# Performance work log

Measured on AMD Instinct MI355X. Metric: run time of the kernel, lower is better.

Reference implementation:

```python
import jax, jax.numpy as jnp
import numpy as np

B, S, D, H, DH = 2, 1024, 1024, 16, 64
SCALE = 1.0 / np.sqrt(DH)


def setup_inputs() -> dict:
    key = jax.random.key(0)
    ks = jax.random.split(key, 9)
    return {
        "x": jax.random.normal(ks[0], (B, S, D), jnp.float32),
        "qkv_w": jax.random.normal(ks[1], (3 * H * DH, D), jnp.float32) * 0.02,
        "out_w": jax.random.normal(ks[2], (D, H * DH), jnp.float32) * 0.02,
        "bias_p": jax.random.uniform(ks[3], (H, 1, 1), jnp.float32) * 2.0,
        "bias_a": jax.random.uniform(ks[4], (H, 1, 1), jnp.float32),
        "mlp_w1": jax.random.normal(ks[5], (H, 2 * H), jnp.float32) * 0.1,
        "mlp_b1": jnp.zeros((H,), jnp.float32),
        "mlp_w2": jax.random.normal(ks[6], (H, H), jnp.float32) * 0.1,
        "mlp_b2": jnp.zeros((H,), jnp.float32),
    }


def reference(x, qkv_w, out_w, bias_p, bias_a, mlp_w1, mlp_b1, mlp_w2, mlp_b2):
    # qkv projection: torch Linear => x @ W.T
    qkv = (x @ qkv_w.T).reshape(B, S, 3, H, DH)
    q = qkv[:, :, 0].transpose(0, 2, 1, 3)  # [B,H,S,DH]
    k = qkv[:, :, 1].transpose(0, 2, 1, 3)
    v = qkv[:, :, 2].transpose(0, 2, 1, 3)

    scores = jnp.einsum('bhqd,bhkd->bhqk', q, k) * SCALE  # [B,H,S,S]

    # Kerple additive bias: -p * log1p(a * |i-j|), per head
    p = jnp.clip(bias_p, 0.01)
    a = jnp.clip(bias_a, 0.01)
    pos = jnp.arange(S, dtype=jnp.float32)
    dist = jnp.abs(pos[None, :] - pos[:, None])  # [S,S]
    kb = -p * jnp.log1p(a * dist)  # [H,S,S]

    # DAPE refinement MLP over per-(i,j) head features
    z = jnp.concatenate(
        [scores, jnp.broadcast_to(kb[None], (B, H, S, S))], axis=1
    ).transpose(0, 2, 3, 1)  # [B,S,S,2H]
    hdn = jax.nn.gelu(z @ mlp_w1.T + mlp_b1, approximate=False)  # [B,S,S,H]
    refine = (hdn @ mlp_w2.T + mlp_b2).transpose(0, 3, 1, 2)  # [B,H,S,S]

    scores = scores + kb[None] + refine
    attn = jax.nn.softmax(scores, axis=-1)  # dropout is identity in eval

    out = jnp.einsum('bhqk,bhkd->bhqd', attn, v)  # [B,H,S,DH]
    out = out.transpose(0, 2, 1, 3).reshape(B, S, H * DH)
    return out @ out_w.T
```

## Files before the change

### kernel.cpp

```cpp
#include <hip/hip_runtime.h>
#include <math.h>

#define Bsz 2
#define Ssz 1024
#define Dsz 1024
#define Hn 16
#define DHsz 64
#define QKV3 3072
#define SCALE 0.125f

typedef __bf16 bf16;
typedef bf16 bf16x8 __attribute__((ext_vector_type(8)));
typedef bf16 bf16x4 __attribute__((ext_vector_type(4)));
typedef float f32x4 __attribute__((ext_vector_type(4)));

#define MFMA(a, b, c) __builtin_amdgcn_mfma_f32_16x16x32_bf16(a, b, c, 0, 0, 0)
#define LDT 72

__global__ void cast_all(const float* __restrict__ x, const float* __restrict__ qw,
                         const float* __restrict__ ow, bf16* __restrict__ xh,
                         bf16* __restrict__ wh, bf16* __restrict__ owh) {
  int idx = (blockIdx.x * 256 + threadIdx.x) * 4;
  const float* src;
  bf16* dst;
  int off = idx;
  if (idx < 2097152) {
    src = x; dst = xh;
  } else if (idx < 2097152 + 3145728) {
    src = qw; dst = wh; off = idx - 2097152;
  } else {
    src = ow; dst = owh; off = idx - (2097152 + 3145728);
  }
  float4 v = *(const float4*)(src + off);
  bf16x4 hv = {(bf16)v.x, (bf16)v.y, (bf16)v.z, (bf16)v.w};
  *(bf16x4*)(dst + off) = hv;
}

__global__ void tk_wfrag(const float* __restrict__ bias_p, const float* __restrict__ bias_a,
                         const float* __restrict__ w1, const float* __restrict__ b1,
                         const float* __restrict__ w2, float2* __restrict__ tk,
                         bf16* __restrict__ wf) {
  if (blockIdx.x == 128) {
    int lane = threadIdx.x;
    if (lane < 64) {
      int l15 = lane & 15, q8 = (lane >> 4) << 3;
      bf16x8 w1d, w2a;
#pragma unroll
      for (int e = 0; e < 8; ++e) {
        int k = q8 + e;
        if (k < 16) {
          w1d[e] = (bf16)w1[l15 * 32 + k];
        } else {
          float w = w1[l15 * 32 + k - 16];
          w1d[e] = (bf16)(w - (float)(bf16)w);
        }
        w2a[e] = (bf16)w2[l15 * 16 + (k & 15)];
      }
      *(bf16x8*)(wf + lane * 8) = w1d;
      *(bf16x8*)(wf + 512 + lane * 8) = w2a;
    }
    return;
  }
  int idx = blockIdx.x * 256 + threadIdx.x;
  int o = idx >> 4, n = idx & 15;
  int d = o - 1024; if (d < 0) d = -d; if (d > 1023) d = 1023;
  float fd = (float)d;
  float t1 = b1[n];
  float t2 = 0.f;
#pragma unroll
  for (int h = 0; h < 16; ++h) {
    float kb = -fmaxf(bias_p[h], 0.01f) * log1pf(fmaxf(bias_a[h], 0.01f) * fd);
    t1 += w1[n * 32 + 16 + h] * kb;
    if (h == n) t2 = kb;
  }
  tk[idx] = make_float2(t1, t2);
}

__global__ __launch_bounds__(256, 3) void k1_qkv(const bf16* __restrict__ A,
                                                 const bf16* __restrict__ B,
                                                 bf16* __restrict__ C) {
  __shared__ __align__(16) bf16 sA[128 * LDT];
  __shared__ __align__(16) bf16 sB[96 * LDT];
  const int tid = threadIdx.x;
  const int lane = tid & 63, wv = tid >> 6;
  const int wr = wv >> 1, wc = wv & 1;
  const int l15 = lane & 15, q8 = (lane >> 4) << 3, q4 = (lane >> 4) << 2;
  const int m0 = blockIdx.y * 128, n0 = blockIdx.x * 96;
  const int r0 = tid >> 3, c8 = (tid & 7) << 3;

  f32x4 acc[4][3];
#pragma unroll
  for (int t = 0; t < 4; ++t)
#pragma unroll
    for (int u = 0; u < 3; ++u)
#pragma unroll
      for (int r = 0; r < 4; ++r) acc[t][u][r] = 0.f;

  bf16x8 rA[4], rB[3];
#define K1_LOAD(kt)                                                         \
  {                                                                         \
    _Pragma("unroll") for (int c = 0; c < 4; ++c)                           \
      rA[c] = *(const bf16x8*)(A + (size_t)(m0 + c * 32 + r0) * Dsz + (kt) + c8);  \
    _Pragma("unroll") for (int c = 0; c < 3; ++c)                           \
      rB[c] = *(const bf16x8*)(B + (size_t)(n0 + c * 32 + r0) * Dsz + (kt) + c8);  \
  }

  K1_LOAD(0)
  for (int kt = 0; kt < Dsz; kt += 64) {
    __syncthreads();
#pragma unroll
    for (int c = 0; c < 4; ++c) *(bf16x8*)&sA[(c * 32 + r0) * LDT + c8] = rA[c];
#pragma unroll
    for (int c = 0; c < 3; ++c) *(bf16x8*)&sB[(c * 32 + r0) * LDT + c8] = rB[c];
    __syncthreads();
    if (kt + 64 < Dsz) K1_LOAD(kt + 64)
#pragma unroll
    for (int ks = 0; ks < 64; ks += 32) {
      bf16x8 fa[4], fb[3];
#pragma unroll
      for (int t = 0; t < 4; ++t)
        fa[t] = *(const bf16x8*)&sA[(wr * 64 + t * 16 + l15) * LDT + ks + q8];
#pragma unroll
      for (int u = 0; u < 3; ++u)
        fb[u] = *(const bf16x8*)&sB[(wc * 48 + u * 16 + l15) * LDT + ks + q8];
#pragma unroll
      for (int t = 0; t < 4; ++t)
#pragma unroll
        for (int u = 0; u < 3; ++u) acc[t][u] = MFMA(fa[t], fb[u], acc[t][u]);
    }
  }
#undef K1_LOAD

#define K1BST 104
  bf16* sBounce = sA;
#pragma unroll
  for (int t = 0; t < 4; ++t) {
    __syncthreads();
#pragma unroll
    for (int u = 0; u < 3; ++u) {
      int col = wc * 48 + u * 16 + l15;
#pragma unroll
      for (int r = 0; r < 4; ++r)
        sBounce[(wr * 16 + q4 + r) * K1BST + col] = (bf16)acc[t][u][r];
    }
    __syncthreads();
    int lr = tid >> 3;
    int grow = m0 + (lr < 16 ? t * 16 + lr : 64 + t * 16 + (lr - 16));
#pragma unroll
    for (int cg = 0; cg < 3; ++cg) {
      int cc = cg * 32 + (tid & 7) * 4;
      bf16x4 vv = *(const bf16x4*)&sBounce[lr * K1BST + cc];
      *(bf16x4*)(C + (size_t)grow * QKV3 + n0 + cc) = vv;
    }
  }
#undef K1BST
}

__global__ void pack_vt(const bf16* __restrict__ qkv, bf16* __restrict__ vt) {
  __shared__ __align__(16) bf16 T[64 * LDT];
  const int tid = threadIdx.x;
  const int bh = blockIdx.y, b = bh >> 4, h = bh & 15;
  const int j0 = blockIdx.x * 64;
#pragma unroll
  for (int c = 0; c < 2; ++c) {
    int lin = c * 256 + tid;
    int jr = lin >> 3, d8 = (lin & 7) << 3;
    bf16x8 v = *(const bf16x8*)(qkv + (size_t)(b * Ssz + j0 + jr) * QKV3 + 2048 + h * DHsz + d8);
#pragma unroll
    for (int e = 0; e < 8; ++e) T[(d8 + e) * LDT + jr] = v[e];
  }
  __syncthreads();
#pragma unroll
  for (int c = 0; c < 2; ++c) {
    int lin = c * 256 + tid;
    int d = lin >> 3, j8 = (lin & 7) << 3;
    bf16x8 o = *(const bf16x8*)&T[d * LDT + j8];
    *(bf16x8*)(vt + ((size_t)(b * Hn + h) * DHsz + d) * Ssz + j0 + j8) = o;
  }
}

__global__ __launch_bounds__(256, 3) void k2_qk(const bf16* __restrict__ qkv,
                                                bf16* __restrict__ scores) {
  __shared__ __align__(16) bf16 sA[128 * LDT], sB[128 * LDT];
  const int tid = threadIdx.x;
  const int lane = tid & 63, wv = tid >> 6;
  const int wr = wv >> 1, wc = wv & 1;
  const int l15 = lane & 15, q8 = (lane >> 4) << 3, q4 = (lane >> 4) << 2;
  const int z = blockIdx.z, b = z >> 4, h = z & 15;
  const int i0 = blockIdx.y * 128, j0 = blockIdx.x * 128;
  const bf16* Ab = qkv + (size_t)b * Ssz * QKV3 + h * DHsz;
  const bf16* Bb = Ab + Ssz;
  const int r0 = tid >> 3, c8 = (tid & 7) << 3;
#pragma unroll
  for (int c = 0; c < 4; ++c) {
    int row = c * 32 + r0;
    *(bf16x8*)&sA[row * LDT + c8] = *(const bf16x8*)(Ab + (size_t)(i0 + row) * QKV3 + c8);
    *(bf16x8*)&sB[row * LDT + c8] = *(const bf16x8*)(Bb + (size_t)(j0 + row) * QKV3 + c8);
  }
  __syncthreads();
  f32x4 acc[4][4];
#pragma unroll
  for (int t = 0; t < 4; ++t)
#pragma unroll
    for (int u = 0; u < 4; ++u)
#pragma unroll
      for (int r = 0; r < 4; ++r) acc[t][u][r] = 0.f;
#pragma unroll
  for (int ks = 0; ks < 64; ks += 32) {
    bf16x8 fa[4], fb[4];
#pragma unroll
    for (int t = 0; t < 4; ++t) fa[t] = *(const bf16x8*)&sA[(wr * 64 + t * 16 + l15) * LDT + ks + q8];
#pragma unroll
    for (int u = 0; u < 4; ++u) fb[u] = *(const bf16x8*)&sB[(wc * 64 + u * 16 + l15) * LDT + ks + q8];
#pragma unroll
    for (int t = 0; t < 4; ++t)
#pragma unroll
      for (int u = 0; u < 4; ++u) acc[t][u] = MFMA(fa[t], fb[u], acc[t][u]);
  }

#define K2BST 136
  bf16* sBounce = sA;
  bf16* dstp = scores + ((size_t)(b * Hn + h) << 20);
#pragma unroll
  for (int t = 0; t < 4; ++t) {
    __syncthreads();
#pragma unroll
    for (int u = 0; u < 4; ++u) {
      int col = wc * 64 + u * 16 + l15;
#pragma unroll
      for (int r = 0; r < 4; ++r)
        sBounce[(wr * 16 + q4 + r) * K2BST + col] = (bf16)(acc[t][u][r] * SCALE);
    }
    __syncthreads();
#pragma unroll
    for (int hf = 0; hf < 2; ++hf) {
      int lr = hf * 16 + (tid >> 4);
      int cc = (tid & 15) * 8;
      bf16x8 vv = *(const bf16x8*)&sBounce[lr * K2BST + cc];
      int grow = i0 + (lr < 16 ? t * 16 + lr : 64 + t * 16 + (lr - 16));
      *(bf16x8*)(dstp + ((size_t)grow << 10) + j0 + cc) = vv;
    }
  }
#undef K2BST
}

__device__ __forceinline__ float gelu_fast(float x) {
  float z = fabsf(x) * 0.70710678118654752f;
  float t = __builtin_amdgcn_rcpf(fmaf(0.47047f, z, 1.0f));
  float poly = t * fmaf(t, fmaf(t, 0.7478556f, -0.0958798f), 0.3480242f);
  float erfa = 1.0f - poly * __expf(-z * z);
  float erfs = copysignf(erfa, x);
  return 0.5f * x * (1.0f + erfs);
}

#define SHS 264

__global__ __launch_bounds__(256, 8) void dape_softmax(bf16* scores,
                                                       const float2* __restrict__ tk,
                                                       const bf16* __restrict__ wf,
                                                       const float* __restrict__ b2,
                                                       float* __restrict__ sums) {
  const int c = blockIdx.x;
  const int i = blockIdx.y;
  const int b = blockIdx.z;
  const int tid = threadIdx.x;
  const int lane = tid & 63, wv = tid >> 6;
  const int l15 = lane & 15, q = lane >> 4;
  const int q8 = q << 3, q4 = q << 2;

  __shared__ bf16 sH[Hn][SHS];
  __shared__ __align__(16) bf16 hdnS[4][2][16][40];
  __shared__ float sumLDS[4][16];

  const bf16x8 w1d = *(const bf16x8*)(wf + lane * 8);
  const bf16x8 w2a = *(const bf16x8*)(wf + 512 + lane * 8);
  const float bias2 = b2[l15];

  if (lane < 32) {
    int row = lane >> 1, col = 16 + (lane & 1) * 8;
    *(bf16x8*)&hdnS[wv][0][row][col] = (bf16x8){};
    *(bf16x8*)&hdnS[wv][1][row][col] = (bf16x8){};
  }

  const int jw = wv * 64;
  bf16* srow = scores + ((size_t)(b * Hn) << 20) + ((size_t)i << 10) + c * 256;
#pragma unroll
  for (int t = 0; t < 2; ++t) {
    int h = t * 8 + (lane >> 3);
    int col = jw + (lane & 7) * 8;
    *(bf16x8*)&sH[h][col] = *(const bf16x8*)(srow + ((size_t)h << 20) + col);
  }

  const float2* tkp = tk + ((size_t)(c * 256 + jw + q4 - i + 1024) << 4) + l15;
  bf16* prow = srow + ((size_t)l15 << 20) + jw;
  float psum = 0.f;

#pragma unroll
  for (int jt = 0; jt < 4; ++jt) {
    const int j0c = jw + jt * 16;
    bf16x8 a1;
#pragma unroll
    for (int e = 0; e < 8; ++e) a1[e] = sH[(q8 + e) & 15][j0c + l15];
    float2 tkv[4];
#pragma unroll
    for (int r = 0; r < 4; ++r) tkv[r] = tkp[jt * 256 + r * 16];
    f32x4 c1 = {tkv[0].x, tkv[1].x, tkv[2].x, tkv[3].x};
    c1 = MFMA(a1, w1d, c1);
#pragma unroll
    for (int r = 0; r < 4; ++r) hdnS[wv][jt & 1][q4 + r][l15] = (bf16)gelu_fast(c1[r]);
    bf16x8 a2 = *(const bf16x8*)&hdnS[wv][jt & 1][l15][q8];
    f32x4 c2 = {bias2, bias2, bias2, bias2};
    c2 = MFMA(a2, w2a, c2);
    bf16x4 sc4 = *(const bf16x4*)&sH[l15][j0c + q4];
    f32x4 pv;
#pragma unroll
    for (int r = 0; r < 4; ++r) {
      float lg = (float)sc4[r] + tkv[r].y + c2[r];
      pv[r] = __expf(lg);
      psum += pv[r];
    }
    bf16x4 p4 = {(bf16)pv[0], (bf16)pv[1], (bf16)pv[2], (bf16)pv[3]};
    *(bf16x4*)(prow + jt * 16 + q4) = p4;
  }

  psum += __shfl_xor(psum, 16, 64);
  psum += __shfl_xor(psum, 32, 64);
  if (lane < 16) sumLDS[wv][lane] = psum;
  __syncthreads();
  if (tid < 16) {
    float tot = sumLDS[0][tid] + sumLDS[1][tid] + sumLDS[2][tid] + sumLDS[3][tid];
    sums[((((b << 10) + i) << 4) + tid) * 4 + c] = tot;
  }
}

__global__ __launch_bounds__(256, 6) void k4_av(const bf16* __restrict__ attn,
                                                const bf16* __restrict__ vt,
                                                const float* __restrict__ sums,
                                                bf16* __restrict__ aout) {
  __shared__ __align__(16) bf16 sA[64 * LDT], sB[64 * LDT];
  const int tid = threadIdx.x;
  const int lane = tid & 63, wv = tid >> 6;
  const int wr = wv >> 1, wc = wv & 1;
  const int l15 = lane & 15, q8 = (lane >> 4) << 3, q4 = (lane >> 4) << 2;
  const int i0 = blockIdx.x * 64, h = blockIdx.y, b = blockIdx.z;
  const bf16* Ab = attn + ((size_t)(b * Hn + h) << 20) + ((size_t)i0 << 10);
  const bf16* Bb = vt + (size_t)(b * Hn + h) * DHsz * Ssz;
  const int r0 = tid >> 3, c8 = (tid & 7) << 3;
  f32x4 acc[2][2];
#pragma unroll
  for (int t = 0; t < 2; ++t)
#pragma unroll
    for (int u = 0; u < 2; ++u)
#pragma unroll
      for (int r = 0; r < 4; ++r) acc[t][u][r] = 0.f;
  bf16x8 rA[2], rB[2];
#define K4_LOAD(kt)                                               \
  {                                                               \
    _Pragma("unroll") for (int c = 0; c < 2; ++c) {               \
      int row = c * 32 + r0;                                      \
      rA[c] = *(const bf16x8*)(Ab + ((size_t)row << 10) + (kt) + c8); \
      rB[c] = *(const bf16x8*)(Bb + ((size_t)row << 10) + (kt) + c8); \
    }                                                             \
  }
  K4_LOAD(0)
  for (int kt = 0; kt < Ssz; kt += 64) {
    __syncthreads();
#pragma unroll
    for (int c = 0; c < 2; ++c) {
      int row = c * 32 + r0;
      *(bf16x8*)&sA[row * LDT + c8] = rA[c];
      *(bf16x8*)&sB[row * LDT + c8] = rB[c];
    }
    __syncthreads();
    if (kt + 64 < Ssz) K4_LOAD(kt + 64)
#pragma unroll
    for (int ks = 0; ks < 64; ks += 32) {
      bf16x8 fa[2], fb[2];
#pragma unroll
      for (int t = 0; t < 2; ++t) fa[t] = *(const bf16x8*)&sA[(wr * 32 + t * 16 + l15) * LDT + ks + q8];
#pragma unroll
      for (int u = 0; u < 2; ++u) fb[u] = *(const bf16x8*)&sB[(wc * 32 + u * 16 + l15) * LDT + ks + q8];
#pragma unroll
      for (int t = 0; t < 2; ++t)
#pragma unroll
        for (int u = 0; u < 2; ++u) acc[t][u] = MFMA(fa[t], fb[u], acc[t][u]);
    }
  }
#undef K4_LOAD

  bf16* sBounce = sA;
  __syncthreads();
#pragma unroll
  for (int t = 0; t < 2; ++t)
#pragma unroll
    for (int r = 0; r < 4; ++r) {
      int lr = wr * 32 + t * 16 + q4 + r;
      int row = i0 + lr;
      f32x4 sv = *(const f32x4*)&sums[((((b << 10) + row) << 4) + h) * 4];
      float inv = 1.f / (sv[0] + sv[1] + sv[2] + sv[3]);
#pragma unroll
      for (int u = 0; u < 2; ++u)
        sBounce[lr * LDT + wc * 32 + u * 16 + l15] = (bf16)(acc[t][u][r] * inv);
    }
  __syncthreads();
#pragma unroll
  for (int r2 = 0; r2 < 2; ++r2) {
    int lr = r2 * 32 + (tid >> 3);
    int cc = (tid & 7) * 8;
    bf16x8 vv = *(const bf16x8*)&sBounce[lr * LDT + cc];
    *(bf16x8*)(aout + (size_t)(b * Ssz + i0 + lr) * Dsz + h * DHsz + cc) = vv;
  }
}

__global__ __launch_bounds__(256, 6) void k5_out(const bf16* __restrict__ A,
                                                 const bf16* __restrict__ B,
                                                 float* __restrict__ C) {
  __shared__ __align__(16) bf16 sA[64 * LDT], sB[64 * LDT];
  const int tid = threadIdx.x;
  const int lane = tid & 63, wv = tid >> 6;
  const int wr = wv >> 1, wc = wv & 1;
  const int l15 = lane & 15, q8 = (lane >> 4) << 3, q4 = (lane >> 4) << 2;
  const int m0 = blockIdx.y * 64, n0 = blockIdx.x * 64;
  const int r0 = tid >> 3, c8 = (tid & 7) << 3;
  f32x4 acc[2][2];
#pragma unroll
  for (int t = 0; t < 2; ++t)
#pragma unroll
    for (int u = 0; u < 2; ++u)
#pragma unroll
      for (int r = 0; r < 4; ++r) acc[t][u][r] = 0.f;
  bf16x8 rA[2], rB[2];
#define K5_LOAD(kt)                                                       \
  {                                                                       \
    _Pragma("unroll") for (int c = 0; c < 2; ++c) {                       \
      int row = c * 32 + r0;                                              \
      rA[c] = *(const bf16x8*)(A + (size_t)(m0 + row) * Dsz + (kt) + c8);   \
      rB[c] = *(const bf16x8*)(B + (size_t)(n0 + row) * Dsz + (kt) + c8);   \
    }                                                                     \
  }
  K5_LOAD(0)
  for (int kt = 0; kt < Dsz; kt += 64) {
    __syncthreads();
#pragma unroll
    for (int c = 0; c < 2; ++c) {
      int row = c * 32 + r0;
      *(bf16x8*)&sA[row * LDT + c8] = rA[c];
      *(bf16x8*)&sB[row * LDT + c8] = rB[c];
    }
    __syncthreads();
    if (kt + 64 < Dsz) K5_LOAD(kt + 64)
#pragma unroll
    for (int ks = 0; ks < 64; ks += 32) {
      bf16x8 fa[2], fb[2];
#pragma unroll
      for (int t = 0; t < 2; ++t) fa[t] = *(const bf16x8*)&sA[(wr * 32 + t * 16 + l15) * LDT + ks + q8];
#pragma unroll
      for (int u = 0; u < 2; ++u) fb[u] = *(const bf16x8*)&sB[(wc * 32 + u * 16 + l15) * LDT + ks + q8];
#pragma unroll
      for (int t = 0; t < 2; ++t)
#pragma unroll
        for (int u = 0; u < 2; ++u) acc[t][u] = MFMA(fa[t], fb[u], acc[t][u]);
    }
  }
#pragma unroll
  for (int t = 0; t < 2; ++t)
#pragma unroll
    for (int u = 0; u < 2; ++u) {
      int col = n0 + wc * 32 + u * 16 + l15;
#pragma unroll
      for (int r = 0; r < 4; ++r) {
        int row = m0 + wr * 32 + t * 16 + q4 + r;
        C[(size_t)row * Dsz + col] = acc[t][u][r];
      }
    }
#undef K5_LOAD
}

extern "C" void kernel_launch(void* const* d_in, const int* in_sizes, int n_in,
                              void* d_out, int out_size, void* d_ws, size_t ws_size,
                              hipStream_t stream) {
  const float* x      = (const float*)d_in[0];
  const float* qkv_w  = (const float*)d_in[1];
  const float* out_w  = (const float*)d_in[2];
  const float* bias_p = (const float*)d_in[3];
  const float* bias_a = (const float*)d_in[4];
  const float* w1     = (const float*)d_in[5];
  const float* b1     = (const float*)d_in[6];
  const float* w2     = (const float*)d_in[7];
  const float* b2     = (const float*)d_in[8];
  float* out = (float*)d_out;

  char* ws = (char*)d_ws;
  const size_t MB = 1ull << 20;
  bf16* ow_h   = (bf16*)(ws + 0 * MB);
  bf16* qkv_bf = (bf16*)(ws + 2 * MB);
  bf16* v_t    = (bf16*)(ws + 14 * MB);
  bf16* aout   = (bf16*)(ws + 18 * MB);
  float* sums  = (float*)(ws + 22 * MB + 65536);
  bf16* wf     = (bf16*)(ws + 22 * MB + 589824);
  float2* tk   = (float2*)(ws + 22 * MB + 655360);
  bf16* x_h    = (bf16*)(ws + 23 * MB);
  bf16* w_h    = (bf16*)(ws + 27 * MB);
  bf16* sc_bf  = (bf16*)(ws + 23 * MB);

  cast_all<<<6144, 256, 0, stream>>>(x, qkv_w, out_w, x_h, w_h, ow_h);
  tk_wfrag<<<129, 256, 0, stream>>>(bias_p, bias_a, w1, b1, w2, tk, wf);

  k1_qkv<<<dim3(QKV3 / 96, (Bsz * Ssz) / 128), 256, 0, stream>>>(x_h, w_h, qkv_bf);
  pack_vt<<<dim3(Ssz / 64, Bsz * Hn), 256, 0, stream>>>(qkv_bf, v_t);

  k2_qk<<<dim3(Ssz / 128, Ssz / 128, Bsz * Hn), 256, 0, stream>>>(qkv_bf, sc_bf);
  dape_softmax<<<dim3(4, Ssz, Bsz), 256, 0, stream>>>(sc_bf, tk, wf, b2, sums);
  k4_av<<<dim3(Ssz / 64, Hn, Bsz), 256, 0, stream>>>(sc_bf, v_t, sums, aout);

  k5_out<<<dim3(Dsz / 64, (Bsz * Ssz) / 64), 256, 0, stream>>>(aout, ow_h, out);
}
```

Baseline: 202.7 us.

## Stage GEMM tiles via direct global-to-LDS loads and widen QKV tile to 128

Replaces the register-staged prefetch in the QKV, QK, AV and output GEMMs with global_load_lds intrinsics that write straight into unpadded 64-wide LDS tiles. The QKV GEMM tile also grows from 128x96 to 128x128, and its epilogue stores 8-wide vectors. This drops the register round trip and the explicit LDS stores. In exchange, the register double-buffering that overlapped the next load with the MFMAs is lost, and the unpadded stride-64 layout may cause LDS bank conflicts on fragment reads.

```diff
diff --git a/kernel.cpp b/kernel.cpp
--- a/kernel.cpp
+++ b/kernel.cpp
@@ -15,7 +15,14 @@
 typedef float f32x4 __attribute__((ext_vector_type(4)));
 
 #define MFMA(a, b, c) __builtin_amdgcn_mfma_f32_16x16x32_bf16(a, b, c, 0, 0, 0)
-#define LDT 72
+
+__device__ __forceinline__ void gstage(const bf16* g, size_t ldg, bf16* ldsbase,
+                                       int lane) {
+  __builtin_amdgcn_global_load_lds(
+      (const __attribute__((address_space(1))) void*)(g + (size_t)(lane >> 3) * ldg +
+                                                      ((lane & 7) << 3)),
+      (__attribute__((address_space(3))) void*)ldsbase, 16, 0, 0);
+}
 
 __global__ void cast_all(const float* __restrict__ x, const float* __restrict__ qw,
                          const float* __restrict__ ow, bf16* __restrict__ xh,
@@ -79,83 +86,73 @@
 __global__ __launch_bounds__(256, 3) void k1_qkv(const bf16* __restrict__ A,
                                                  const bf16* __restrict__ B,
                                                  bf16* __restrict__ C) {
-  __shared__ __align__(16) bf16 sA[128 * LDT];
-  __shared__ __align__(16) bf16 sB[96 * LDT];
+  __shared__ __align__(16) bf16 sA[128 * 64];
+  __shared__ __align__(16) bf16 sB[128 * 64];
   const int tid = threadIdx.x;
   const int lane = tid & 63, wv = tid >> 6;
   const int wr = wv >> 1, wc = wv & 1;
   const int l15 = lane & 15, q8 = (lane >> 4) << 3, q4 = (lane >> 4) << 2;
-  const int m0 = blockIdx.y * 128, n0 = blockIdx.x * 96;
-  const int r0 = tid >> 3, c8 = (tid & 7) << 3;
-
-  f32x4 acc[4][3];
+  const int m0 = blockIdx.y * 128, n0 = blockIdx.x * 128;
+
+  f32x4 acc[4][4];
 #pragma unroll
   for (int t = 0; t < 4; ++t)
 #pragma unroll
-    for (int u = 0; u < 3; ++u)
+    for (int u = 0; u < 4; ++u)
 #pragma unroll
       for (int r = 0; r < 4; ++r) acc[t][u][r] = 0.f;
 
-  bf16x8 rA[4], rB[3];
-#define K1_LOAD(kt)                                                         \
-  {                                                                         \
-    _Pragma("unroll") for (int c = 0; c < 4; ++c)                           \
-      rA[c] = *(const bf16x8*)(A + (size_t)(m0 + c * 32 + r0) * Dsz + (kt) + c8);  \
-    _Pragma("unroll") for (int c = 0; c < 3; ++c)                           \
-      rB[c] = *(const bf16x8*)(B + (size_t)(n0 + c * 32 + r0) * Dsz + (kt) + c8);  \
-  }
-
-  K1_LOAD(0)
   for (int kt = 0; kt < Dsz; kt += 64) {
     __syncthreads();
 #pragma unroll
-    for (int c = 0; c < 4; ++c) *(bf16x8*)&sA[(c * 32 + r0) * LDT + c8] = rA[c];
-#pragma unroll
-    for (int c = 0; c < 3; ++c) *(bf16x8*)&sB[(c * 32 + r0) * LDT + c8] = rB[c];
-    __syncthreads();
-    if (kt + 64 < Dsz) K1_LOAD(kt + 64)
+    for (int c = 0; c < 4; ++c) {
+      int row = wv * 32 + c * 8;
+      gstage(A + (size_t)(m0 + row) * Dsz + kt, Dsz, &sA[row * 64], lane);
+      gstage(B + (size_t)(n0 + row) * Dsz + kt, Dsz, &sB[row * 64], lane);
+    }
+    __syncthreads();
 #pragma unroll
     for (int ks = 0; ks < 64; ks += 32) {
-      bf16x8 fa[4], fb[3];
+      bf16x8 fa[4], fb[4];
 #pragma unroll
       for (int t = 0; t < 4; ++t)
-        fa[t] = *(const bf16x8*)&sA[(wr * 64 + t * 16 + l15) * LDT + ks + q8];
-#pragma unroll
-      for (int u = 0; u < 3; ++u)
-        fb[u] = *(const bf16x8*)&sB[(wc * 48 + u * 16 + l15) * LDT + ks + q8];
+        fa[t] = *(const bf16x8*)&sA[(wr * 64 + t * 16 + l15) * 64 + ks + q8];
+#pragma unroll
+      for (int u = 0; u < 4; ++u)
+        fb[u] = *(const bf16x8*)&sB[(wc * 64 + u * 16 + l15) * 64 + ks + q8];
 #pragma unroll
       for (int t = 0; t < 4; ++t)
 #pragma unroll
-        for (int u = 0; u < 3; ++u) acc[t][u] = MFMA(fa[t], fb[u], acc[t][u]);
-    }
-  }
-#undef K1_LOAD
-
-#define K1BST 104
+        for (int u = 0; u < 4; ++u) acc[t][u] = MFMA(fa[t], fb[u], acc[t][u]);
+    }
+  }
+
+#define K1BST 136
   bf16* sBounce = sA;
 #pragma unroll
   for (int t = 0; t < 4; ++t) {
     __syncthreads();
 #pragma unroll
-    for (int u = 0; u < 3; ++u) {
-      int col = wc * 48 + u * 16 + l15;
+    for (int u = 0; u < 4; ++u) {
+      int col = wc * 64 + u * 16 + l15;
 #pragma unroll
       for (int r = 0; r < 4; ++r)
         sBounce[(wr * 16 + q4 + r) * K1BST + col] = (bf16)acc[t][u][r];
     }
     __syncthreads();
-    int lr = tid >> 3;
-    int grow = m0 + (lr < 16 ? t * 16 + lr : 64 + t * 16 + (lr - 16));
-#pragma unroll
-    for (int cg = 0; cg < 3; ++cg) {
-      int cc = cg * 32 + (tid & 7) * 4;
-      bf16x4 vv = *(const bf16x4*)&sBounce[lr * K1BST + cc];
-      *(bf16x4*)(C + (size_t)grow * QKV3 + n0 + cc) = vv;
+#pragma unroll
+    for (int hf = 0; hf < 2; ++hf) {
+      int lr = hf * 16 + (tid >> 4);
+      int cc = (tid & 15) * 8;
+      bf16x8 vv = *(const bf16x8*)&sBounce[lr * K1BST + cc];
+      int grow = m0 + (lr < 16 ? t * 16 + lr : 64 + t * 16 + (lr - 16));
+      *(bf16x8*)(C + (size_t)grow * QKV3 + n0 + cc) = vv;
     }
   }
 #undef K1BST
 }
 
+#define LDT 72
 __global__ void pack_vt(const bf16* __restrict__ qkv, bf16* __restrict__ vt) {
   __shared__ __align__(16) bf16 T[64 * LDT];
   const int tid = threadIdx.x;
@@ -181,7 +178,7 @@
 
 __global__ __launch_bounds__(256, 3) void k2_qk(const bf16* __restrict__ qkv,
                                                 bf16* __restrict__ scores) {
-  __shared__ __align__(16) bf16 sA[128 * LDT], sB[128 * LDT];
+  __shared__ __align__(16) bf16 sA[128 * 64], sB[128 * 64];
   const int tid = threadIdx.x;
   const int lane = tid & 63, wv = tid >> 6;
   const int wr = wv >> 1, wc = wv & 1;
@@ -190,12 +187,11 @@
   const int i0 = blockIdx.y * 128, j0 = blockIdx.x * 128;
   const bf16* Ab = qkv + (size_t)b * Ssz * QKV3 + h * DHsz;
   const bf16* Bb = Ab + Ssz;
-  const int r0 = tid >> 3, c8 = (tid & 7) << 3;
 #pragma unroll
   for (int c = 0; c < 4; ++c) {
-    int row = c * 32 + r0;
-    *(bf16x8*)&sA[row * LDT + c8] = *(const bf16x8*)(Ab + (size_t)(i0 + row) * QKV3 + c8);
-    *(bf16x8*)&sB[row * LDT + c8] = *(const bf16x8*)(Bb + (size_t)(j0 + row) * QKV3 + c8);
+    int row = wv * 32 + c * 8;
+    gstage(Ab + (size_t)(i0 + row) * QKV3, QKV3, &sA[row * 64], lane);
+    gstage(Bb + (size_t)(j0 + row) * QKV3, QKV3, &sB[row * 64], lane);
   }
   __syncthreads();
   f32x4 acc[4][4];
@@ -209,9 +205,9 @@
   for (int ks = 0; ks < 64; ks += 32) {
     bf16x8 fa[4], fb[4];
 #pragma unroll
-    for (int t = 0; t < 4; ++t) fa[t] = *(const bf16x8*)&sA[(wr * 64 + t * 16 + l15) * LDT + ks + q8];
-#pragma unroll
-    for (int u = 0; u < 4; ++u) fb[u] = *(const bf16x8*)&sB[(wc * 64 + u * 16 + l15) * LDT + ks + q8];
+    for (int t = 0; t < 4; ++t) fa[t] = *(const bf16x8*)&sA[(wr * 64 + t * 16 + l15) * 64 + ks + q8];
+#pragma unroll
+    for (int u = 0; u < 4; ++u) fb[u] = *(const bf16x8*)&sB[(wc * 64 + u * 16 + l15) * 64 + ks + q8];
 #pragma unroll
     for (int t = 0; t < 4; ++t)
 #pragma unroll
@@ -337,7 +333,9 @@
                                                 const bf16* __restrict__ vt,
                                                 const float* __restrict__ sums,
                                                 bf16* __restrict__ aout) {
-  __shared__ __align__(16) bf16 sA[64 * LDT], sB[64 * LDT];
+  __shared__ __align__(16) bf16 S[2 * 64 * 64];
+  bf16* sA = S;
+  bf16* sB = S + 64 * 64;
   const int tid = threadIdx.x;
   const int lane = tid & 63, wv = tid >> 6;
   const int wr = wv >> 1, wc = wv & 1;
@@ -345,7 +343,6 @@
   const int i0 = blockIdx.x * 64, h = blockIdx.y, b = blockIdx.z;
   const bf16* Ab = attn + ((size_t)(b * Hn + h) << 20) + ((size_t)i0 << 10);
   const bf16* Bb = vt + (size_t)(b * Hn + h) * DHsz * Ssz;
-  const int r0 = tid >> 3, c8 = (tid & 7) << 3;
   f32x4 acc[2][2];
 #pragma unroll
   for (int t = 0; t < 2; ++t)
@@ -353,42 +350,30 @@
     for (int u = 0; u < 2; ++u)
 #pragma unroll
       for (int r = 0; r < 4; ++r) acc[t][u][r] = 0.f;
-  bf16x8 rA[2], rB[2];
-#define K4_LOAD(kt)                                               \
-  {                                                               \
-    _Pragma("unroll") for (int c = 0; c < 2; ++c) {               \
-      int row = c * 32 + r0;                                      \
-      rA[c] = *(const bf16x8*)(Ab + ((size_t)row << 10) + (kt) + c8); \
-      rB[c] = *(const bf16x8*)(Bb + ((size_t)row << 10) + (kt) + c8); \
-    }                                                             \
-  }
-  K4_LOAD(0)
+
   for (int kt = 0; kt < Ssz; kt += 64) {
     __syncthreads();
 #pragma unroll
     for (int c = 0; c < 2; ++c) {
-      int row = c * 32 + r0;
-      *(bf16x8*)&sA[row * LDT + c8] = rA[c];
-      *(bf16x8*)&sB[row * LDT + c8] = rB[c];
-    }
-    __syncthreads();
-    if (kt + 64 < Ssz) K4_LOAD(kt + 64)
+      int row = wv * 16 + c * 8;
+      gstage(Ab + ((size_t)row << 10) + kt, Ssz, &sA[row * 64], lane);
+      gstage(Bb + ((size_t)row << 10) + kt, Ssz, &sB[row * 64], lane);
+    }
+    __syncthreads();
 #pragma unroll
     for (int ks = 0; ks < 64; ks += 32) {
       bf16x8 fa[2], fb[2];
 #pragma unroll
-      for (int t = 0; t < 2; ++t) fa[t] = *(const bf16x8*)&sA[(wr * 32 + t * 16 + l15) * LDT + ks + q8];
-#pragma unroll
-      for (int u = 0; u < 2; ++u) fb[u] = *(const bf16x8*)&sB[(wc * 32 + u * 16 + l15) * LDT + ks + q8];
+      for (int t = 0; t < 2; ++t) fa[t] = *(const bf16x8*)&sA[(wr * 32 + t * 16 + l15) * 64 + ks + q8];
+#pragma unroll
+      for (int u = 0; u < 2; ++u) fb[u] = *(const bf16x8*)&sB[(wc * 32 + u * 16 + l15) * 64 + ks + q8];
 #pragma unroll
       for (int t = 0; t < 2; ++t)
 #pragma unroll
         for (int u = 0; u < 2; ++u) acc[t][u] = MFMA(fa[t], fb[u], acc[t][u]);
     }
   }
-#undef K4_LOAD
-
-  bf16* sBounce = sA;
+
   __syncthreads();
 #pragma unroll
   for (int t = 0; t < 2; ++t)
@@ -400,14 +385,14 @@
       float inv = 1.f / (sv[0] + sv[1] + sv[2] + sv[3]);
 #pragma unroll
       for (int u = 0; u < 2; ++u)
-        sBounce[lr * LDT + wc * 32 + u * 16 + l15] = (bf16)(acc[t][u][r] * inv);
+        S[lr * LDT + wc * 32 + u * 16 + l15] = (bf16)(acc[t][u][r] * inv);
     }
   __syncthreads();
 #pragma unroll
   for (int r2 = 0; r2 < 2; ++r2) {
     int lr = r2 * 32 + (tid >> 3);
     int cc = (tid & 7) * 8;
-    bf16x8 vv = *(const bf16x8*)&sBounce[lr * LDT + cc];
+    bf16x8 vv = *(const bf16x8*)&S[lr * LDT + cc];
     *(bf16x8*)(aout + (size_t)(b * Ssz + i0 + lr) * Dsz + h * DHsz + cc) = vv;
   }
 }
@@ -415,13 +400,14 @@
 __global__ __launch_bounds__(256, 6) void k5_out(const bf16* __restrict__ A,
                                                  const bf16* __restrict__ B,
                                                  float* __restrict__ C) {
-  __shared__ __align__(16) bf16 sA[64 * LDT], sB[64 * LDT];
+  __shared__ __align__(16) bf16 S[2 * 64 * 64];
+  bf16* sA = S;
+  bf16* sB = S + 64 * 64;
   const int tid = threadIdx.x;
   const int lane = tid & 63, wv = tid >> 6;
   const int wr = wv >> 1, wc = wv & 1;
   const int l15 = lane & 15, q8 = (lane >> 4) << 3, q4 = (lane >> 4) << 2;
   const int m0 = blockIdx.y * 64, n0 = blockIdx.x * 64;
-  const int r0 = tid >> 3, c8 = (tid & 7) << 3;
   f32x4 acc[2][2];
 #pragma unroll
   for (int t = 0; t < 2; ++t)
@@ -429,33 +415,23 @@
     for (int u = 0; u < 2; ++u)
 #pragma unroll
       for (int r = 0; r < 4; ++r) acc[t][u][r] = 0.f;
-  bf16x8 rA[2], rB[2];
-#define K5_LOAD(kt)                                                       \
-  {                                                                       \
-    _Pragma("unroll") for (int c = 0; c < 2; ++c) {                       \
-      int row = c * 32 + r0;                                              \
-      rA[c] = *(const bf16x8*)(A + (size_t)(m0 + row) * Dsz + (kt) + c8);   \
-      rB[c] = *(const bf16x8*)(B + (size_t)(n0 + row) * Dsz + (kt) + c8);   \
-    }                                                                     \
-  }
-  K5_LOAD(0)
+
   for (int kt = 0; kt < Dsz; kt += 64) {
     __syncthreads();
 #pragma unroll
     for (int c = 0; c < 2; ++c) {
-      int row = c * 32 + r0;
-      *(bf16x8*)&sA[row * LDT + c8] = rA[c];
-      *(bf16x8*)&sB[row * LDT + c8] = rB[c];
-    }
-    __syncthreads();
-    if (kt + 64 < Dsz) K5_LOAD(kt + 64)
+      int row = wv * 16 + c * 8;
+      gstage(A + (size_t)(m0 + row) * Dsz + kt, Dsz, &sA[row * 64], lane);
+      gstage(B + (size_t)(n0 + row) * Dsz + kt, Dsz, &sB[row * 64], lane);
+    }
+    __syncthreads();
 #pragma unroll
     for (int ks = 0; ks < 64; ks += 32) {
       bf16x8 fa[2], fb[2];
 #pragma unroll
-      for (int t = 0; t < 2; ++t) fa[t] = *(const bf16x8*)&sA[(wr * 32 + t * 16 + l15) * LDT + ks + q8];
-#pragma unroll
-      for (int u = 0; u < 2; ++u) fb[u] = *(const bf16x8*)&sB[(wc * 32 + u * 16 + l15) * LDT + ks + q8];
+      for (int t = 0; t < 2; ++t) fa[t] = *(const bf16x8*)&sA[(wr * 32 + t * 16 + l15) * 64 + ks + q8];
+#pragma unroll
+      for (int u = 0; u < 2; ++u) fb[u] = *(const bf16x8*)&sB[(wc * 32 + u * 16 + l15) * 64 + ks + q8];
 #pragma unroll
       for (int t = 0; t < 2; ++t)
 #pragma unroll
@@ -473,7 +449,6 @@
         C[(size_t)row * Dsz + col] = acc[t][u][r];
       }
     }
-#undef K5_LOAD
 }
 
 extern "C" void kernel_launch(void* const* d_in, const int* in_sizes, int n_in,
@@ -506,7 +481,7 @@
   cast_all<<<6144, 256, 0, stream>>>(x, qkv_w, out_w, x_h, w_h, ow_h);
   tk_wfrag<<<129, 256, 0, stream>>>(bias_p, bias_a, w1, b1, w2, tk, wf);
 
-  k1_qkv<<<dim3(QKV3 / 96, (Bsz * Ssz) / 128), 256, 0, stream>>>(x_h, w_h, qkv_bf);
+  k1_qkv<<<dim3(QKV3 / 128, (Bsz * Ssz) / 128), 256, 0, stream>>>(x_h, w_h, qkv_bf);
   pack_vt<<<dim3(Ssz / 64, Bsz * Hn), 256, 0, stream>>>(qkv_bf, v_t);
 
   k2_qk<<<dim3(Ssz / 128, Ssz / 128, Bsz * Hn), 256, 0, stream>>>(qkv_bf, sc_bf);
```

Result: slower. 212.4 us (+4.8%).
